# Kernel tuning notes

Measured on AMD Instinct MI355X. Metric: run time of the kernel, lower is better.

The kernel has to match this reference:

```python
import jax, jax.numpy as jnp
import numpy as np


def setup_inputs() -> dict:
    key = jax.random.key(0)
    k1, k2, k3 = jax.random.split(key, 3)
    B, S, H, E = 4, 4096, 7168, 256
    return {
        "hidden_states": jax.random.normal(k1, (B, S, H), dtype=jnp.float32),
        "gate_weight": jax.random.normal(k2, (E, H), dtype=jnp.float32) * (H ** -0.5),
        "bias": jax.random.normal(k3, (E,), dtype=jnp.float32) * 0.01,
        "n_group": 8,
        "topk_group": 4,
        "top_k": 8,
    }


def reference(hidden_states, gate_weight, bias, n_group, topk_group, top_k):
    B, S, H = hidden_states.shape
    E = gate_weight.shape[0]
    group_size = E // n_group
    x = hidden_states.reshape(-1, H)  # [T, H]
    logits = jnp.einsum("th,eh->te", x, gate_weight)  # [T, E]
    scores = jax.nn.sigmoid(logits) + bias  # [T, E]
    scores_g = scores.reshape(-1, n_group, group_size)  # [T, G, E/G]
    group_scores = scores_g.max(axis=-1)  # [T, G]
    _, sel_groups = jax.lax.top_k(group_scores, topk_group)  # [T, topk_group]
    # group mask: 1.0 for selected groups (indices are distinct, so sum of one-hots is 0/1)
    group_mask = jax.nn.one_hot(sel_groups, n_group, dtype=scores.dtype).sum(axis=1)  # [T, G]
    masked = (scores_g * group_mask[:, :, None]).reshape(-1, E)  # [T, E]
    weights, indices = jax.lax.top_k(masked, top_k)  # [T, top_k]
    weights = weights / (weights.sum(axis=-1, keepdims=True) + 1e-6)
    return weights.reshape(B, S, -1), indices.reshape(B, S, -1)
```

## Files before the change

### kernel.cpp

```cpp
#include <hip/hip_runtime.h>


#define TTOK 16384
#define EEXP 256
#define HDIM 7168
#define BM 128
#define BE 128
#define BK 32
#define SPLITK 2
#define KSLICE (HDIM / SPLITK)
#define NSTEP (KSLICE / BK)
#define NTHR 512
#define LDS_BYTES 81920
#define ABASE 49152
#define EPI_LDS (64 * 257 * 4)

typedef __attribute__((ext_vector_type(4))) float f32x4;
typedef __attribute__((ext_vector_type(8))) _Float16 h8;

__device__ __forceinline__ void gload_lds16(const void* g, void* l) {
  typedef const __attribute__((address_space(1))) unsigned int gu32;
  typedef __attribute__((address_space(3))) unsigned int lu32;
  __builtin_amdgcn_global_load_lds((gu32*)g, (lu32*)l, 16, 0, 0);
}

__global__ __launch_bounds__(64) void pack_w_kernel(const float* __restrict__ W,
                                                    _Float16* __restrict__ blob) {
  const int kcg = blockIdx.x;
  const int eb = blockIdx.y;
  const int lane = threadIdx.x;
  const int e = eb * 16 + (lane & 15);
  const int k0 = kcg * 32 + (lane >> 4) * 8;
  const float* src = W + (size_t)e * HDIM + k0;
  h8 hi, lo;
#pragma unroll
  for (int j = 0; j < 8; ++j) {
    float x = src[j];
    _Float16 h = (_Float16)x;
    hi[j] = h;
    lo[j] = (_Float16)((x - (float)h) * 2048.0f);
  }
  const int slice = kcg / NSTEP, kcl = kcg % NSTEP;
  const int ehalf = eb >> 3, ebl = eb & 7;
  char* dst = (char*)blob + ((size_t)(slice * 2 + ehalf) * NSTEP + kcl) * 16384 +
              (ebl * 2) * 1024 + lane * 16;
  *(h8*)dst = hi;
  *(h8*)(dst + 1024) = lo;
}

__global__ __launch_bounds__(NTHR, 4) void gate_kernel(
    const float* __restrict__ X, const _Float16* __restrict__ Wblob,
    float* __restrict__ part) {
  extern __shared__ char smem[];

  const int bid = blockIdx.x;
  const int slice = (bid & 7) >> 2;
  const int ehalf = (bid >> 3) & 1;
  const int tb = ((bid >> 4) << 2) | (bid & 3);
  const int tok0 = tb * BM;
  const int kbase = slice * KSLICE;
  const char* blobs = (const char*)Wblob +
                      ((size_t)(slice * 2 + ehalf) * NSTEP) * 16384;

  const int tid = threadIdx.x;
  const int lane = tid & 63;
  const int wid = tid >> 6;
  const int wr = wid >> 1;
  const int wc = wid & 1;

  f32x4 ra[2];

  f32x4 acc1[2][4], acc2[2][4];
#pragma unroll
  for (int m = 0; m < 2; ++m)
#pragma unroll
    for (int n = 0; n < 4; ++n) {
      acc1[m][n] = (f32x4){0.f, 0.f, 0.f, 0.f};
      acc2[m][n] = (f32x4){0.f, 0.f, 0.f, 0.f};
    }

  auto LOADA = [&](int T) {
    const float* p = X + (size_t)(tok0 + (tid >> 2)) * HDIM + kbase + T * BK +
                     (tid & 3) * 8;
    ra[0] = *(const f32x4*)p;
    ra[1] = *(const f32x4*)(p + 4);
  };

  auto STAGEB = [&](int T, int buf) {
    const char* gs = blobs + (size_t)T * 16384 + lane * 16;
    char* lb = smem + buf * 16384 + lane * 16;
    gload_lds16(gs + (wid * 2) * 1024, lb + (wid * 2) * 1024);
    gload_lds16(gs + (wid * 2 + 1) * 1024, lb + (wid * 2 + 1) * 1024);
  };

  auto STOREA = [&](int buf) {
    h8 hi, lo;
#pragma unroll
    for (int half = 0; half < 2; ++half) {
      const f32x4 v = ra[half];
#pragma unroll
      for (int j = 0; j < 4; ++j) {
        const float x = v[j];
        const _Float16 h = (_Float16)x;
        hi[half * 4 + j] = h;
        lo[half * 4 + j] = (_Float16)((x - (float)h) * 2048.0f);
      }
    }
    char* ah = smem + ABASE + buf * 16384;
    const int row = tid >> 2, q = tid & 3;
    *(h8*)(ah + q * 2048 + row * 16) = hi;
    *(h8*)(ah + 8192 + q * 2048 + row * 16) = lo;
  };

  auto PHASE = [&](int pa, int pb) {
    const char* ahp = smem + ABASE + pa * 16384;
    const char* bb = smem + pb * 16384;
    h8 ah[2], al[2];
#pragma unroll
    for (int m = 0; m < 2; ++m) {
      const int r_ = wr * 32 + m * 16 + (lane & 15);
      const int ao_ = (lane >> 4) * 2048 + r_ * 16;
      ah[m] = *(const h8*)(ahp + ao_);
      al[m] = *(const h8*)(ahp + 8192 + ao_);
    }
    __builtin_amdgcn_s_setprio(1);
#pragma unroll
    for (int n = 0; n < 4; ++n) {
      const int bo_ = ((wc * 4 + n) * 2) * 1024 + lane * 16;
      const h8 bh = *(const h8*)(bb + bo_);
      const h8 bl = *(const h8*)(bb + bo_ + 1024);
#pragma unroll
      for (int m = 0; m < 2; ++m) {
        acc1[m][n] = __builtin_amdgcn_mfma_f32_16x16x32_f16(ah[m], bh, acc1[m][n], 0, 0, 0);
        acc2[m][n] = __builtin_amdgcn_mfma_f32_16x16x32_f16(ah[m], bl, acc2[m][n], 0, 0, 0);
        acc2[m][n] = __builtin_amdgcn_mfma_f32_16x16x32_f16(al[m], bh, acc2[m][n], 0, 0, 0);
      }
    }
    __builtin_amdgcn_s_setprio(0);
  };

  STAGEB(0, 0);
  LOADA(0);
  STAGEB(1, 1);
  STOREA(0);
  LOADA(1);
  asm volatile("s_waitcnt vmcnt(4) lgkmcnt(0)" ::: "memory");
  __builtin_amdgcn_s_barrier();

  int pa = 0, pb = 0;
#pragma unroll 1
  for (int T = 0; T < NSTEP; ++T) {
    const bool p2 = (T + 2 < NSTEP);
    if (p2) {
      int sb = pb + 2;
      if (sb >= 3) sb -= 3;
      STAGEB(T + 2, sb);
    }
    PHASE(pa, pb);
    if (T + 1 < NSTEP) {
      STOREA(pa ^ 1);
      if (p2) LOADA(T + 2);
      if (p2)
        asm volatile("s_waitcnt vmcnt(4) lgkmcnt(0)" ::: "memory");
      else
        asm volatile("s_waitcnt vmcnt(0) lgkmcnt(0)" ::: "memory");
      __builtin_amdgcn_s_barrier();
    }
    pa ^= 1;
    pb = (pb == 2) ? 0 : pb + 1;
  }

  float* pbase = part + ((size_t)slice * TTOK + tok0) * EEXP + ehalf * BE;
#pragma unroll
  for (int m = 0; m < 2; ++m)
#pragma unroll
    for (int n = 0; n < 4; ++n) {
      const int e = wc * 64 + n * 16 + (lane & 15);
      const int t0 = wr * 32 + m * 16 + (lane >> 4) * 4;
#pragma unroll
      for (int r = 0; r < 4; ++r)
        pbase[(size_t)(t0 + r) * EEXP + e] =
            acc1[m][n][r] + acc2[m][n][r] * (1.0f / 2048.0f);
    }
}

__global__ __launch_bounds__(256) void epilogue_kernel(
    const float* __restrict__ part, const float* __restrict__ bias,
    float* __restrict__ outw, float* __restrict__ outi) {
  extern __shared__ float sc[];
  const int tid = threadIdx.x;
  const long t0 = (long)blockIdx.x * 64;

  const int e4 = (tid & 63) * 4;
  const int rsub = tid >> 6;
  const f32x4 bv = *(const f32x4*)(bias + e4);
#pragma unroll
  for (int rr = 0; rr < 16; ++rr) {
    const int row = rr * 4 + rsub;
    const f32x4 a = *(const f32x4*)(part + (t0 + row) * EEXP + e4);
    const f32x4 c = *(const f32x4*)(part + ((long)TTOK + t0 + row) * EEXP + e4);
#pragma unroll
    for (int j = 0; j < 4; ++j) {
      const float v = a[j] + c[j];
      sc[row * 257 + e4 + j] = 1.0f / (1.0f + expf(-v)) + bv[j];
    }
  }
  __syncthreads();

  if (tid < 64) {
    const float* s = sc + tid * 257;
    float gmax[8];
#pragma unroll
    for (int g = 0; g < 8; ++g) {
      float mx = -1e30f;
      for (int j = 0; j < 32; ++j) mx = fmaxf(mx, s[g * 32 + j]);
      gmax[g] = mx;
    }
    unsigned selmask = 0;
    for (int it = 0; it < 4; ++it) {
      float best = -1e30f;
      int bi = 0;
      for (int g = 0; g < 8; ++g)
        if (!((selmask >> g) & 1) && gmax[g] > best) {
          best = gmax[g];
          bi = g;
        }
      selmask |= 1u << bi;
    }
    float vals[8];
    int idx[8];
#pragma unroll
    for (int j = 0; j < 8; ++j) {
      vals[j] = -1e30f;
      idx[j] = 0;
    }
    for (int e = 0; e < 256; ++e) {
      const float v = ((selmask >> (e >> 5)) & 1) ? s[e] : 0.0f;
      if (v > vals[7]) {
        int p = 7;
        while (p > 0 && v > vals[p - 1]) {
          vals[p] = vals[p - 1];
          idx[p] = idx[p - 1];
          --p;
        }
        vals[p] = v;
        idx[p] = e;
      }
    }
    float ssum = 0.0f;
#pragma unroll
    for (int j = 0; j < 8; ++j) ssum += vals[j];
    const float den = ssum + 1e-6f;
    const long tg = t0 + tid;
#pragma unroll
    for (int j = 0; j < 8; ++j) {
      outw[tg * 8 + j] = vals[j] / den;
      outi[tg * 8 + j] = (float)idx[j];
    }
  }
}

extern "C" void kernel_launch(void* const* d_in, const int* in_sizes, int n_in,
                              void* d_out, int out_size, void* d_ws, size_t ws_size,
                              hipStream_t stream) {
  const float* X = (const float*)d_in[0];
  const float* W = (const float*)d_in[1];
  const float* bias = (const float*)d_in[2];

  _Float16* wblob = (_Float16*)d_ws;
  float* part = (float*)((char*)d_ws + (size_t)EEXP * HDIM * 4);

  float* outw = (float*)d_out;
  float* outi = outw + (size_t)TTOK * 8;

  hipFuncSetAttribute((const void*)gate_kernel,
                      hipFuncAttributeMaxDynamicSharedMemorySize, LDS_BYTES);
  hipFuncSetAttribute((const void*)epilogue_kernel,
                      hipFuncAttributeMaxDynamicSharedMemorySize, EPI_LDS);

  pack_w_kernel<<<dim3(HDIM / 32, EEXP / 16), 64, 0, stream>>>(W, wblob);
  gate_kernel<<<SPLITK * 2 * (TTOK / BM), NTHR, LDS_BYTES, stream>>>(X, wblob, part);
  epilogue_kernel<<<TTOK / 64, 256, EPI_LDS, stream>>>(part, bias, outw, outi);
}
```

Before: 292.2 us.

## Halve threads per block and double per-warp tile to 64x64

Drops the gate GEMM block from 512 to 256 threads, so each of the 4 warps computes a 64x64 output tile (4x4 MFMA fragments) instead of 32x64. Global loads, LDS staging and the vmcnt wait counts are rescaled to match. In PHASE all B fragments are now loaded up front and the MFMAs are reordered into two batches for better issue density. The aim is more register reuse of A/B fragments per LDS read, at the cost of doubled accumulator registers and lower occupancy (launch bound min blocks 2).

```diff
diff --git a/kernel.cpp b/kernel.cpp
--- a/kernel.cpp
+++ b/kernel.cpp
@@ -10,7 +10,7 @@
 #define SPLITK 2
 #define KSLICE (HDIM / SPLITK)
 #define NSTEP (KSLICE / BK)
-#define NTHR 512
+#define NTHR 256
 #define LDS_BYTES 81920
 #define ABASE 49152
 #define EPI_LDS (64 * 257 * 4)
@@ -48,7 +48,7 @@
   *(h8*)(dst + 1024) = lo;
 }
 
-__global__ __launch_bounds__(NTHR, 4) void gate_kernel(
+__global__ __launch_bounds__(NTHR, 2) void gate_kernel(
     const float* __restrict__ X, const _Float16* __restrict__ Wblob,
     float* __restrict__ part) {
   extern __shared__ char smem[];
@@ -68,11 +68,11 @@
   const int wr = wid >> 1;
   const int wc = wid & 1;
 
-  f32x4 ra[2];
-
-  f32x4 acc1[2][4], acc2[2][4];
-#pragma unroll
-  for (int m = 0; m < 2; ++m)
+  f32x4 ra[4];
+
+  f32x4 acc1[4][4], acc2[4][4];
+#pragma unroll
+  for (int m = 0; m < 4; ++m)
 #pragma unroll
     for (int n = 0; n < 4; ++n) {
       acc1[m][n] = (f32x4){0.f, 0.f, 0.f, 0.f};
@@ -80,62 +80,76 @@
     }
 
   auto LOADA = [&](int T) {
-    const float* p = X + (size_t)(tok0 + (tid >> 2)) * HDIM + kbase + T * BK +
-                     (tid & 3) * 8;
-    ra[0] = *(const f32x4*)p;
-    ra[1] = *(const f32x4*)(p + 4);
+    const float* p = X + (size_t)(tok0 + (tid >> 1)) * HDIM + kbase + T * BK +
+                     (tid & 1) * 16;
+#pragma unroll
+    for (int i = 0; i < 4; ++i) ra[i] = *(const f32x4*)(p + i * 4);
   };
 
   auto STAGEB = [&](int T, int buf) {
     const char* gs = blobs + (size_t)T * 16384 + lane * 16;
     char* lb = smem + buf * 16384 + lane * 16;
-    gload_lds16(gs + (wid * 2) * 1024, lb + (wid * 2) * 1024);
-    gload_lds16(gs + (wid * 2 + 1) * 1024, lb + (wid * 2 + 1) * 1024);
+#pragma unroll
+    for (int i = 0; i < 4; ++i) {
+      const int gb = wid * 4 + i;
+      gload_lds16(gs + gb * 1024, lb + gb * 1024);
+    }
   };
 
   auto STOREA = [&](int buf) {
-    h8 hi, lo;
-#pragma unroll
-    for (int half = 0; half < 2; ++half) {
-      const f32x4 v = ra[half];
-#pragma unroll
-      for (int j = 0; j < 4; ++j) {
-        const float x = v[j];
-        const _Float16 h = (_Float16)x;
-        hi[half * 4 + j] = h;
-        lo[half * 4 + j] = (_Float16)((x - (float)h) * 2048.0f);
+    const int row = tid >> 1, qb = (tid & 1) * 2;
+    char* ah = smem + ABASE + buf * 16384;
+#pragma unroll
+    for (int c = 0; c < 2; ++c) {
+      h8 hi, lo;
+#pragma unroll
+      for (int half = 0; half < 2; ++half) {
+        const f32x4 v = ra[2 * c + half];
+#pragma unroll
+        for (int j = 0; j < 4; ++j) {
+          const float x = v[j];
+          const _Float16 h = (_Float16)x;
+          hi[half * 4 + j] = h;
+          lo[half * 4 + j] = (_Float16)((x - (float)h) * 2048.0f);
+        }
       }
-    }
-    char* ah = smem + ABASE + buf * 16384;
-    const int row = tid >> 2, q = tid & 3;
-    *(h8*)(ah + q * 2048 + row * 16) = hi;
-    *(h8*)(ah + 8192 + q * 2048 + row * 16) = lo;
+      const int off = (qb + c) * 2048 + row * 16;
+      *(h8*)(ah + off) = hi;
+      *(h8*)(ah + 8192 + off) = lo;
+    }
   };
 
   auto PHASE = [&](int pa, int pb) {
     const char* ahp = smem + ABASE + pa * 16384;
     const char* bb = smem + pb * 16384;
-    h8 ah[2], al[2];
-#pragma unroll
-    for (int m = 0; m < 2; ++m) {
-      const int r_ = wr * 32 + m * 16 + (lane & 15);
+    h8 ah[4], al[4];
+#pragma unroll
+    for (int m = 0; m < 4; ++m) {
+      const int r_ = wr * 64 + m * 16 + (lane & 15);
       const int ao_ = (lane >> 4) * 2048 + r_ * 16;
       ah[m] = *(const h8*)(ahp + ao_);
       al[m] = *(const h8*)(ahp + 8192 + ao_);
     }
-    __builtin_amdgcn_s_setprio(1);
+    h8 bh[4], bl[4];
 #pragma unroll
     for (int n = 0; n < 4; ++n) {
       const int bo_ = ((wc * 4 + n) * 2) * 1024 + lane * 16;
-      const h8 bh = *(const h8*)(bb + bo_);
-      const h8 bl = *(const h8*)(bb + bo_ + 1024);
-#pragma unroll
-      for (int m = 0; m < 2; ++m) {
-        acc1[m][n] = __builtin_amdgcn_mfma_f32_16x16x32_f16(ah[m], bh, acc1[m][n], 0, 0, 0);
-        acc2[m][n] = __builtin_amdgcn_mfma_f32_16x16x32_f16(ah[m], bl, acc2[m][n], 0, 0, 0);
-        acc2[m][n] = __builtin_amdgcn_mfma_f32_16x16x32_f16(al[m], bh, acc2[m][n], 0, 0, 0);
+      bh[n] = *(const h8*)(bb + bo_);
+      bl[n] = *(const h8*)(bb + bo_ + 1024);
+    }
+    __builtin_amdgcn_s_setprio(1);
+#pragma unroll
+    for (int n = 0; n < 4; ++n)
+#pragma unroll
+      for (int m = 0; m < 4; ++m) {
+        acc1[m][n] = __builtin_amdgcn_mfma_f32_16x16x32_f16(ah[m], bh[n], acc1[m][n], 0, 0, 0);
+        acc2[m][n] = __builtin_amdgcn_mfma_f32_16x16x32_f16(ah[m], bl[n], acc2[m][n], 0, 0, 0);
       }
-    }
+#pragma unroll
+    for (int n = 0; n < 4; ++n)
+#pragma unroll
+      for (int m = 0; m < 4; ++m)
+        acc2[m][n] = __builtin_amdgcn_mfma_f32_16x16x32_f16(al[m], bh[n], acc2[m][n], 0, 0, 0);
     __builtin_amdgcn_s_setprio(0);
   };
 
@@ -144,7 +158,7 @@
   STAGEB(1, 1);
   STOREA(0);
   LOADA(1);
-  asm volatile("s_waitcnt vmcnt(4) lgkmcnt(0)" ::: "memory");
+  asm volatile("s_waitcnt vmcnt(8) lgkmcnt(0)" ::: "memory");
   __builtin_amdgcn_s_barrier();
 
   int pa = 0, pb = 0;
@@ -161,7 +175,7 @@
       STOREA(pa ^ 1);
       if (p2) LOADA(T + 2);
       if (p2)
-        asm volatile("s_waitcnt vmcnt(4) lgkmcnt(0)" ::: "memory");
+        asm volatile("s_waitcnt vmcnt(8) lgkmcnt(0)" ::: "memory");
       else
         asm volatile("s_waitcnt vmcnt(0) lgkmcnt(0)" ::: "memory");
       __builtin_amdgcn_s_barrier();
@@ -172,11 +186,11 @@
 
   float* pbase = part + ((size_t)slice * TTOK + tok0) * EEXP + ehalf * BE;
 #pragma unroll
-  for (int m = 0; m < 2; ++m)
+  for (int m = 0; m < 4; ++m)
 #pragma unroll
     for (int n = 0; n < 4; ++n) {
       const int e = wc * 64 + n * 16 + (lane & 15);
-      const int t0 = wr * 32 + m * 16 + (lane >> 4) * 4;
+      const int t0 = wr * 64 + m * 16 + (lane >> 4) * 4;
 #pragma unroll
       for (int r = 0; r < 4; ++r)
         pbase[(size_t)(t0 + r) * EEXP + e] =
```

After: 297.6 us. Within noise of the previous version (+1.9%).
